# Kernel optimization log

Hardware: AMD Instinct MI355X
Metric: run time of the kernel (lower is better)

Reference implementation:

```python
import jax, jax.numpy as jnp
import numpy as np

B, N, TOKEN_DIM, HIDDEN = 4, 2048, 512, 128
LN_EPS = 1e-5
NEG_SLOPE = 0.01  # torch LeakyReLU default


def setup_inputs() -> dict:
    key = jax.random.key(0)
    ks = jax.random.split(key, 6)
    s_fc = 1.0 / np.sqrt(TOKEN_DIM)
    s_at = 1.0 / np.sqrt(2 * HIDDEN)
    return {
        "token_embedding": jax.random.normal(ks[0], (B, N, TOKEN_DIM), jnp.float32),
        "fc_w": jax.random.uniform(ks[1], (HIDDEN, TOKEN_DIM), jnp.float32, -s_fc, s_fc),
        "fc_b": jax.random.uniform(ks[2], (HIDDEN,), jnp.float32, -s_fc, s_fc),
        "attn_w": jax.random.uniform(ks[3], (1, 2 * HIDDEN), jnp.float32, -s_at, s_at),
        "attn_b": jax.random.uniform(ks[4], (1,), jnp.float32, -s_at, s_at),
        "ln_g": jnp.ones((HIDDEN,), jnp.float32),
        "ln_b": jnp.zeros((HIDDEN,), jnp.float32),
    }


def reference(token_embedding, fc_w, fc_b, attn_w, attn_b, ln_g, ln_b):
    # h = LayerNorm(Linear(x))  -> [B, N, H]
    h = jnp.einsum("bnt,ht->bnh", token_embedding, fc_w) + fc_b
    mu = jnp.mean(h, axis=-1, keepdims=True)
    var = jnp.mean(jnp.square(h - mu), axis=-1, keepdims=True)
    h = ln_g * (h - mu) * jax.lax.rsqrt(var + LN_EPS) + ln_b

    # Original: concat_h[b,i,j] = [h[b,j], h[b,i]] then attn_fc (dropout is identity at eval).
    # Algebraically: score[b,i,j] = h[b,j].w_row + h[b,i].w_col + bias
    w_row = attn_w[0, :HIDDEN]
    w_col = attn_w[0, HIDDEN:]
    s_row = h @ w_row  # [B, N]
    s_col = h @ w_col  # [B, N]
    e = s_col[:, :, None] + s_row[:, None, :] + attn_b[0]  # [B, N, N]
    e = jnp.where(e >= 0, e, NEG_SLOPE * e)  # LeakyReLU
    a = jax.nn.softmax(e, axis=-1)
    h_prime = jnp.einsum("bij,bjh->bih", a, h)
    return h_prime
```

## Files before the change

kernel.cpp:

```cpp
#include <hip/hip_runtime.h>

#define NB      4
#define NTOK    2048
#define TOKDIM  512
#define HID     128
#define NROWS   (NB * NTOK)
#define LN_EPS  1e-5f
#define NEG_SLOPE 0.01f

typedef short bf16x8 __attribute__((ext_vector_type(8)));
typedef float f32x4  __attribute__((ext_vector_type(4)));

static __device__ __forceinline__ unsigned short f2bf(float f) {
    union { float f; unsigned int i; } v; v.f = f;
    unsigned int i = v.i;
    i += 0x7FFFu + ((i >> 16) & 1u);
    return (unsigned short)(i >> 16);
}

__global__ __launch_bounds__(256) void k_cvtw(const float* __restrict__ W,
                                              unsigned short* __restrict__ Wbf) {
    const int g = (blockIdx.x * 256 + threadIdx.x) * 4;
    float4 v = *(const float4*)(W + g);
    ushort4 o;
    o.x = f2bf(v.x); o.y = f2bf(v.y); o.z = f2bf(v.z); o.w = f2bf(v.w);
    *(ushort4*)(Wbf + g) = o;
}

__global__ __launch_bounds__(512) void k_fused(const float* __restrict__ X,
                                               const unsigned short* __restrict__ Wbf,
                                               const float* __restrict__ fcb,
                                               const float* __restrict__ attnw,
                                               const float* __restrict__ attnb,
                                               const float* __restrict__ lng,
                                               const float* __restrict__ lnb,
                                               unsigned short* __restrict__ hT,
                                               float* __restrict__ srow,
                                               float* __restrict__ cc) {
    __shared__ char smem[16640 + 16 * 132 * 4];
    unsigned short* ldsX = (unsigned short*)smem;
    unsigned short* ldsT = (unsigned short*)smem;
    float* hfull = (float*)(smem + 16640);

    const int tid  = threadIdx.x;
    const int wv   = tid >> 6;
    const int lane = tid & 63;
    const int m    = lane & 15;
    const int q    = lane >> 4;
    const int rowbase = blockIdx.x * 16;
    const int nbase   = wv * 16;

    {
        const int r  = tid >> 5;
        const int c0 = (tid & 31) * 16;
        const float* xp = X + (size_t)(rowbase + r) * TOKDIM + c0;
        bf16x8 v0, v1;
#pragma unroll
        for (int u = 0; u < 8; ++u) v0[u] = (short)f2bf(xp[u]);
#pragma unroll
        for (int u = 0; u < 8; ++u) v1[u] = (short)f2bf(xp[8 + u]);
        *(bf16x8*)&ldsX[r * 520 + c0]     = v0;
        *(bf16x8*)&ldsX[r * 520 + c0 + 8] = v1;
    }
    __syncthreads();

    const unsigned short* wp = Wbf + (size_t)(nbase + m) * TOKDIM + q * 8;
    f32x4 acc = {0.f, 0.f, 0.f, 0.f};
#pragma unroll
    for (int kk = 0; kk < TOKDIM / 32; ++kk) {
        bf16x8 a = *(const bf16x8*)&ldsX[m * 520 + kk * 32 + q * 8];
        bf16x8 b = *(const bf16x8*)(wp + kk * 32);
        acc = __builtin_amdgcn_mfma_f32_16x16x32_bf16(a, b, acc, 0, 0, 0);
    }

    {
        const float bias = fcb[nbase + m];
#pragma unroll
        for (int r = 0; r < 4; ++r)
            hfull[(q * 4 + r) * 132 + nbase + m] = acc[r] + bias;
    }
    __syncthreads();

    {
        const int r   = tid >> 5;
        const int l32 = tid & 31;
        const int c0  = l32 * 4;
        float4 hv = *(const float4*)&hfull[r * 132 + c0];
        float v[4] = {hv.x, hv.y, hv.z, hv.w};

        float s  = v[0] + v[1] + v[2] + v[3];
        float ss = v[0]*v[0] + v[1]*v[1] + v[2]*v[2] + v[3]*v[3];
#pragma unroll
        for (int d = 1; d < 32; d <<= 1) {
            s  += __shfl_xor(s,  d, 64);
            ss += __shfl_xor(ss, d, 64);
        }
        float mu  = s * (1.f / HID);
        float var = ss * (1.f / HID) - mu * mu;
        float rs  = rsqrtf(var + LN_EPS);

        float n[4], sr = 0.f, sc = 0.f;
#pragma unroll
        for (int k = 0; k < 4; ++k) {
            n[k] = lng[c0 + k] * (v[k] - mu) * rs + lnb[c0 + k];
            sr += n[k] * attnw[c0 + k];
            sc += n[k] * attnw[HID + c0 + k];
            ldsT[(c0 + k) * 20 + r] = f2bf(n[k]);
        }
#pragma unroll
        for (int d = 1; d < 32; d <<= 1) {
            sr += __shfl_xor(sr, d, 64);
            sc += __shfl_xor(sc, d, 64);
        }
        if (l32 == 0) {
            int grow = rowbase + r;
            srow[grow] = sr;
            cc[grow]   = sc + attnb[0];
        }
    }
    __syncthreads();

    {
        const int d  = tid >> 2;
        const int j4 = (tid & 3) * 4;
        const int b    = blockIdx.x >> 7;
        const int jblk = (blockIdx.x & 127) * 16;
        ushort4 o;
        o.x = ldsT[d * 20 + j4 + 0];
        o.y = ldsT[d * 20 + j4 + 1];
        o.z = ldsT[d * 20 + j4 + 2];
        o.w = ldsT[d * 20 + j4 + 3];
        *(ushort4*)(hT + ((size_t)(b * HID + d)) * NTOK + jblk + j4) = o;
    }
}

__global__ __launch_bounds__(512) void k_attn(const unsigned short* __restrict__ hT,
                                              const float* __restrict__ srow,
                                              const float* __restrict__ cc,
                                              float* __restrict__ out) {
    __shared__ unsigned short pP[32][264];
    __shared__ float pDen[32][16];
    __shared__ float denv[32];

    const int tid  = threadIdx.x;
    const int wv   = tid >> 6;
    const int lane = tid & 63;
    const int m    = lane & 15;
    const int q    = lane >> 4;
    const int rowbase = blockIdx.x * 32;
    const int b    = blockIdx.x >> 6;
    const int dbase = wv * 16;

    const int i_loc = tid >> 4;
    const int jseg  = (tid & 15) * 16;
    const float ci  = cc[rowbase + i_loc];
    const float* sp = srow + (size_t)b * NTOK + jseg;

    const unsigned short* hp =
        hT + ((size_t)(b * HID + dbase + m)) * NTOK + q * 8;

    f32x4 acc0 = {0.f, 0.f, 0.f, 0.f};
    f32x4 acc1 = {0.f, 0.f, 0.f, 0.f};
    float lsum = 0.f;

    for (int ch = 0; ch < 8; ++ch) {
        {
            const float* s0 = sp + ch * 256;
            bf16x8 v0, v1;
#pragma unroll
            for (int u = 0; u < 8; ++u) {
                float z = ci + s0[u];
                z = fmaxf(z, NEG_SLOPE * z);
                float p = __expf(z);
                lsum += p;
                v0[u] = (short)f2bf(p);
            }
#pragma unroll
            for (int u = 0; u < 8; ++u) {
                float z = ci + s0[8 + u];
                z = fmaxf(z, NEG_SLOPE * z);
                float p = __expf(z);
                lsum += p;
                v1[u] = (short)f2bf(p);
            }
            *(bf16x8*)&pP[i_loc][jseg]     = v0;
            *(bf16x8*)&pP[i_loc][jseg + 8] = v1;
        }
        __syncthreads();

#pragma unroll
        for (int s = 0; s < 8; ++s) {
            bf16x8 bfr = *(const bf16x8*)(hp + ch * 256 + s * 32);
            bf16x8 a0  = *(const bf16x8*)&pP[m][s * 32 + q * 8];
            bf16x8 a1  = *(const bf16x8*)&pP[16 + m][s * 32 + q * 8];
            acc0 = __builtin_amdgcn_mfma_f32_16x16x32_bf16(a0, bfr, acc0, 0, 0, 0);
            acc1 = __builtin_amdgcn_mfma_f32_16x16x32_bf16(a1, bfr, acc1, 0, 0, 0);
        }
        __syncthreads();
    }

    pDen[i_loc][tid & 15] = lsum;
    __syncthreads();
    if (tid < 32) {
        float d = 0.f;
#pragma unroll
        for (int k = 0; k < 16; ++k) d += pDen[tid][k];
        denv[tid] = 1.f / d;
    }
    __syncthreads();

#pragma unroll
    for (int r = 0; r < 4; ++r) {
        int r0 = q * 4 + r;
        out[(size_t)(rowbase + r0) * HID + dbase + m]      = acc0[r] * denv[r0];
        out[(size_t)(rowbase + 16 + r0) * HID + dbase + m] = acc1[r] * denv[16 + r0];
    }
}

extern "C" void kernel_launch(void* const* d_in, const int* in_sizes, int n_in,
                              void* d_out, int out_size, void* d_ws, size_t ws_size,
                              hipStream_t stream) {
    const float* X     = (const float*)d_in[0];
    const float* W     = (const float*)d_in[1];
    const float* fcb   = (const float*)d_in[2];
    const float* attnw = (const float*)d_in[3];
    const float* attnb = (const float*)d_in[4];
    const float* lng   = (const float*)d_in[5];
    const float* lnb   = (const float*)d_in[6];
    float* out = (float*)d_out;

    char* ws = (char*)d_ws;
    unsigned short* hT   = (unsigned short*)ws;
    float*          srow = (float*)(ws + 2u * 1024 * 1024);
    float*          cchd = (float*)(ws + 2u * 1024 * 1024 + 32u * 1024);
    unsigned short* Wbf  = (unsigned short*)(ws + 2u * 1024 * 1024 + 64u * 1024);

    k_cvtw <<<64,  256, 0, stream>>>(W, Wbf);
    k_fused<<<NROWS / 16, 512, 0, stream>>>(X, Wbf, fcb, attnw, attnb, lng, lnb,
                                            hT, srow, cchd);
    k_attn <<<NROWS / 32, 512, 0, stream>>>(hT, srow, cchd, out);
}
```

Measured before the change: 114.5 us.

## Drop weight-convert kernel and double-buffer attention P tiles with register prefetch

Removes the separate fp32-to-bf16 weight conversion launch and instead converts W to bf16 inline while loading the B operand in the fused linear/LayerNorm kernel. In the attention kernel, the probability tile in shared memory is double-buffered, and the next chunk's srow values and hT fragments are prefetched into registers. This removes one barrier per chunk and overlaps global loads with the MFMA work. It costs more registers and extra redundant conversion of W in every block.

```diff
diff --git a/kernel.cpp b/kernel.cpp
--- a/kernel.cpp
+++ b/kernel.cpp
@@ -18,17 +18,19 @@
     return (unsigned short)(i >> 16);
 }
 
-__global__ __launch_bounds__(256) void k_cvtw(const float* __restrict__ W,
-                                              unsigned short* __restrict__ Wbf) {
-    const int g = (blockIdx.x * 256 + threadIdx.x) * 4;
-    float4 v = *(const float4*)(W + g);
-    ushort4 o;
-    o.x = f2bf(v.x); o.y = f2bf(v.y); o.z = f2bf(v.z); o.w = f2bf(v.w);
-    *(ushort4*)(Wbf + g) = o;
+static __device__ __forceinline__ bf16x8 cvt8(const float* __restrict__ p) {
+    float4 a = *(const float4*)(p);
+    float4 b = *(const float4*)(p + 4);
+    bf16x8 r;
+    r[0] = (short)f2bf(a.x); r[1] = (short)f2bf(a.y);
+    r[2] = (short)f2bf(a.z); r[3] = (short)f2bf(a.w);
+    r[4] = (short)f2bf(b.x); r[5] = (short)f2bf(b.y);
+    r[6] = (short)f2bf(b.z); r[7] = (short)f2bf(b.w);
+    return r;
 }
 
 __global__ __launch_bounds__(512) void k_fused(const float* __restrict__ X,
-                                               const unsigned short* __restrict__ Wbf,
+                                               const float* __restrict__ W,
                                                const float* __restrict__ fcb,
                                                const float* __restrict__ attnw,
                                                const float* __restrict__ attnb,
@@ -64,12 +66,12 @@
     }
     __syncthreads();
 
-    const unsigned short* wp = Wbf + (size_t)(nbase + m) * TOKDIM + q * 8;
+    const float* wp = W + (size_t)(nbase + m) * TOKDIM + q * 8;
     f32x4 acc = {0.f, 0.f, 0.f, 0.f};
 #pragma unroll
     for (int kk = 0; kk < TOKDIM / 32; ++kk) {
         bf16x8 a = *(const bf16x8*)&ldsX[m * 520 + kk * 32 + q * 8];
-        bf16x8 b = *(const bf16x8*)(wp + kk * 32);
+        bf16x8 b = cvt8(wp + kk * 32);
         acc = __builtin_amdgcn_mfma_f32_16x16x32_bf16(a, b, acc, 0, 0, 0);
     }
 
@@ -138,7 +140,7 @@
                                               const float* __restrict__ srow,
                                               const float* __restrict__ cc,
                                               float* __restrict__ out) {
-    __shared__ unsigned short pP[32][264];
+    __shared__ unsigned short pP[2][32][264];
     __shared__ float pDen[32][16];
     __shared__ float denv[32];
 
@@ -163,13 +165,23 @@
     f32x4 acc1 = {0.f, 0.f, 0.f, 0.f};
     float lsum = 0.f;
 
+    float4 s0 = *(const float4*)(sp);
+    float4 s1 = *(const float4*)(sp + 4);
+    float4 s2 = *(const float4*)(sp + 8);
+    float4 s3 = *(const float4*)(sp + 12);
+    bf16x8 bcur[8], bnxt[8];
+#pragma unroll
+    for (int s = 0; s < 8; ++s) bcur[s] = *(const bf16x8*)(hp + s * 32);
+
+#pragma unroll
     for (int ch = 0; ch < 8; ++ch) {
         {
-            const float* s0 = sp + ch * 256;
+            float sv[16] = {s0.x, s0.y, s0.z, s0.w, s1.x, s1.y, s1.z, s1.w,
+                            s2.x, s2.y, s2.z, s2.w, s3.x, s3.y, s3.z, s3.w};
             bf16x8 v0, v1;
 #pragma unroll
             for (int u = 0; u < 8; ++u) {
-                float z = ci + s0[u];
+                float z = ci + sv[u];
                 z = fmaxf(z, NEG_SLOPE * z);
                 float p = __expf(z);
                 lsum += p;
@@ -177,26 +189,39 @@
             }
 #pragma unroll
             for (int u = 0; u < 8; ++u) {
-                float z = ci + s0[8 + u];
+                float z = ci + sv[8 + u];
                 z = fmaxf(z, NEG_SLOPE * z);
                 float p = __expf(z);
                 lsum += p;
                 v1[u] = (short)f2bf(p);
             }
-            *(bf16x8*)&pP[i_loc][jseg]     = v0;
-            *(bf16x8*)&pP[i_loc][jseg + 8] = v1;
-        }
+            *(bf16x8*)&pP[ch & 1][i_loc][jseg]     = v0;
+            *(bf16x8*)&pP[ch & 1][i_loc][jseg + 8] = v1;
+        }
+
+        if (ch < 7) {
+            const float* spn = sp + (ch + 1) * 256;
+            s0 = *(const float4*)(spn);
+            s1 = *(const float4*)(spn + 4);
+            s2 = *(const float4*)(spn + 8);
+            s3 = *(const float4*)(spn + 12);
+            const unsigned short* hpn = hp + (ch + 1) * 256;
+#pragma unroll
+            for (int s = 0; s < 8; ++s) bnxt[s] = *(const bf16x8*)(hpn + s * 32);
+        }
+
         __syncthreads();
 
 #pragma unroll
         for (int s = 0; s < 8; ++s) {
-            bf16x8 bfr = *(const bf16x8*)(hp + ch * 256 + s * 32);
-            bf16x8 a0  = *(const bf16x8*)&pP[m][s * 32 + q * 8];
-            bf16x8 a1  = *(const bf16x8*)&pP[16 + m][s * 32 + q * 8];
-            acc0 = __builtin_amdgcn_mfma_f32_16x16x32_bf16(a0, bfr, acc0, 0, 0, 0);
-            acc1 = __builtin_amdgcn_mfma_f32_16x16x32_bf16(a1, bfr, acc1, 0, 0, 0);
-        }
-        __syncthreads();
+            bf16x8 a0 = *(const bf16x8*)&pP[ch & 1][m][s * 32 + q * 8];
+            bf16x8 a1 = *(const bf16x8*)&pP[ch & 1][16 + m][s * 32 + q * 8];
+            acc0 = __builtin_amdgcn_mfma_f32_16x16x32_bf16(a0, bcur[s], acc0, 0, 0, 0);
+            acc1 = __builtin_amdgcn_mfma_f32_16x16x32_bf16(a1, bcur[s], acc1, 0, 0, 0);
+        }
+
+#pragma unroll
+        for (int s = 0; s < 8; ++s) bcur[s] = bnxt[s];
     }
 
     pDen[i_loc][tid & 15] = lsum;
@@ -233,10 +258,8 @@
     unsigned short* hT   = (unsigned short*)ws;
     float*          srow = (float*)(ws + 2u * 1024 * 1024);
     float*          cchd = (float*)(ws + 2u * 1024 * 1024 + 32u * 1024);
-    unsigned short* Wbf  = (unsigned short*)(ws + 2u * 1024 * 1024 + 64u * 1024);
-
-    k_cvtw <<<64,  256, 0, stream>>>(W, Wbf);
-    k_fused<<<NROWS / 16, 512, 0, stream>>>(X, Wbf, fcb, attnw, attnb, lng, lnb,
+
+    k_fused<<<NROWS / 16, 512, 0, stream>>>(X, W, fcb, attnw, attnb, lng, lnb,
                                             hT, srow, cchd);
     k_attn <<<NROWS / 32, 512, 0, stream>>>(hT, srow, cchd, out);
 }
```

New measurement: 110.2 us. 3.8% less time.
